# Kernel optimization log

Measured on AMD Instinct MI355X. Metric: run time of the kernel, lower is better.

Reference implementation:

```python
import jax, jax.numpy as jnp
import numpy as np

B, T, D, H, HD, I = 256, 1, 2048, 16, 128, 5504
EPS = 1e-6
ROPE_THETA = 10000.0


def setup_inputs() -> dict:
    key = jax.random.key(0)
    ks = jax.random.split(key, 20)
    W = 0.02  # weight init scale
    hidden_states = jax.random.normal(ks[0], (B, T, D), jnp.float32)
    # RoPE tables for each batch element at a distinct decode position
    pos = jnp.arange(B, dtype=jnp.float32) % 4096.0
    inv_freq = 1.0 / (ROPE_THETA ** (jnp.arange(0, HD, 2, dtype=jnp.float32) / HD))
    ang = pos[:, None] * inv_freq[None, :]                      # [B, HD/2]
    emb = jnp.concatenate([ang, ang], axis=-1)                  # [B, HD]
    cos = jnp.cos(emb)[:, None, :]                              # [B, 1, HD]
    sin = jnp.sin(emb)[:, None, :]
    n = lambda k, s: jax.random.normal(k, s, jnp.float32) * W
    return {
        'hidden_states': hidden_states, 'cos': cos, 'sin': sin,
        'router_w': n(ks[1], (D,)), 'router_b': jnp.zeros((1,), jnp.float32),
        'ln1_w': jnp.ones((D,), jnp.float32), 'ln2_w': jnp.ones((D,), jnp.float32),
        'wq': n(ks[2], (D, D)), 'bq': jnp.zeros((D,), jnp.float32),
        'wk': n(ks[3], (D, D)), 'bk': jnp.zeros((D,), jnp.float32),
        'wv': n(ks[4], (D, D)), 'bv': jnp.zeros((D,), jnp.float32),
        'wo': n(ks[5], (D, D)),
        'w_gate': n(ks[6], (D, I)), 'w_up': n(ks[7], (D, I)), 'w_down': n(ks[8], (I, D)),
        'k_sel': 128,
    }


def _rms(x, w):
    v = jnp.mean(jnp.square(x), axis=-1, keepdims=True)
    return x * jax.lax.rsqrt(v + EPS) * w


def _rotate_half(x):
    x1, x2 = jnp.split(x, 2, axis=-1)
    return jnp.concatenate([-x2, x1], axis=-1)


def _decoder_layer(x, cs, sn, ln1_w, ln2_w, wq, bq, wk, bk, wv, bv, wo, w_gate, w_up, w_down):
    # x: [k, T, D]; cs/sn: [k, T, HD]
    k = x.shape[0]
    h = _rms(x, ln1_w)
    q = (h @ wq + bq).reshape(k, T, H, HD).transpose(0, 2, 1, 3)  # [k,H,T,HD]
    kk = (h @ wk + bk).reshape(k, T, H, HD).transpose(0, 2, 1, 3)
    v = (h @ wv + bv).reshape(k, T, H, HD).transpose(0, 2, 1, 3)
    c = cs[:, None, :, :]  # [k,1,T,HD]
    s = sn[:, None, :, :]
    q = q * c + _rotate_half(q) * s
    kk = kk * c + _rotate_half(kk) * s
    att = jnp.einsum('bhqd,bhkd->bhqk', q, kk) * (HD ** -0.5)
    p = jax.nn.softmax(att, axis=-1)  # T==1: trivial causal mask
    o = jnp.einsum('bhqk,bhkd->bhqd', p, v).transpose(0, 2, 1, 3).reshape(k, T, D) @ wo
    x = x + o
    h2 = _rms(x, ln2_w)
    mlp = (jax.nn.silu(h2 @ w_gate) * (h2 @ w_up)) @ w_down
    return x + mlp


def reference(hidden_states, cos, sin, router_w, router_b, ln1_w, ln2_w,
              wq, bq, wk, bk, wv, bv, wo, w_gate, w_up, w_down, k_sel):
    # causal router: linear D->1 scores per batch row (T==1 decode step)
    scores = hidden_states[:, 0, :] @ router_w + router_b[0]   # [B]
    probs = jax.nn.sigmoid(scores)
    _, sel_idx = jax.lax.top_k(probs, k_sel)                   # [k]
    x_sel = hidden_states[sel_idx]                             # gather [k,T,D]
    cs, sn = cos[sel_idx], sin[sel_idx]                        # [k,T,HD]
    x_out = _decoder_layer(x_sel, cs, sn, ln1_w, ln2_w, wq, bq, wk, bk,
                           wv, bv, wo, w_gate, w_up, w_down)
    return hidden_states.at[sel_idx].set(x_out)                # scatter back
```

## Files before the change

kernel.cpp:

```cpp
#include <hip/hip_runtime.h>
#include <hip/hip_bf16.h>
#include <stdint.h>


#define D_ 2048
#define I_ 5504
#define NROWS 256
#define KSEL 128

typedef __attribute__((ext_vector_type(8))) short short8;
typedef __attribute__((ext_vector_type(4))) float floatx4;

__device__ __forceinline__ unsigned int pk2(float lo, float hi) {
  __hip_bfloat162 h = __float22bfloat162_rn(float2{lo, hi});
  unsigned int u; __builtin_memcpy(&u, &h, 4); return u;
}

__global__ void k_zero(float4* __restrict__ p, int n4) {
  int i = blockIdx.x * 256 + threadIdx.x;
  int st = gridDim.x * 256;
  for (; i < n4; i += st) p[i] = float4{0.f, 0.f, 0.f, 0.f};
}

__global__ void k_router(const float* __restrict__ hid, const float* __restrict__ rw,
                         const float* __restrict__ rb, float* __restrict__ scores) {
  int b = blockIdx.x, t = threadIdx.x;
  const float4* x4 = (const float4*)(hid + (size_t)b * D_);
  const float4* w4 = (const float4*)rw;
  float s = 0.f;
#pragma unroll
  for (int c = 0; c < 2; ++c) {
    float4 xv = x4[t + c * 256], wv = w4[t + c * 256];
    s += xv.x * wv.x + xv.y * wv.y + xv.z * wv.z + xv.w * wv.w;
  }
  for (int o = 32; o; o >>= 1) s += __shfl_down(s, o);
  __shared__ float red[4];
  if ((t & 63) == 0) red[t >> 6] = s;
  __syncthreads();
  if (t == 0) scores[b] = red[0] + red[1] + red[2] + red[3] + rb[0];
}

__global__ void k_select(const float* __restrict__ scores, const int* __restrict__ kptr,
                         int* __restrict__ sel, int* __restrict__ pos) {
  __shared__ float sv[NROWS];
  int t = threadIdx.x;
  sv[t] = scores[t];
  __syncthreads();
  float s = sv[t];
  int c = 0;
  for (int j = 0; j < NROWS; ++j) {
    float o = sv[j];
    c += (o > s) || (o == s && j < t);
  }
  int k = *kptr;
  if (c < k) sel[c] = t;
  pos[t] = (c < k) ? c : -1;
}

__global__ void k_rms1(const float* __restrict__ hid, const int* __restrict__ sel,
                       const float* __restrict__ ln1, const float* __restrict__ bv,
                       unsigned short* __restrict__ Hb, float* __restrict__ V,
                       float* __restrict__ X1) {
  int i = blockIdx.x, t = threadIdx.x;
  int r = sel[i];
  const float4* x4 = (const float4*)(hid + (size_t)r * D_);
  float4 xa = x4[2 * t], xb = x4[2 * t + 1];
  float ss = xa.x * xa.x + xa.y * xa.y + xa.z * xa.z + xa.w * xa.w
           + xb.x * xb.x + xb.y * xb.y + xb.z * xb.z + xb.w * xb.w;
  for (int o = 32; o; o >>= 1) ss += __shfl_down(ss, o);
  __shared__ float red[4];
  if ((t & 63) == 0) red[t >> 6] = ss;
  __syncthreads();
  float inv = rsqrtf((red[0] + red[1] + red[2] + red[3]) * (1.0f / D_) + 1e-6f);
  const float4* w4 = (const float4*)ln1;
  float4 wa = w4[2 * t], wb = w4[2 * t + 1];
  union { unsigned int u[4]; uint4 q; } pk;
  pk.u[0] = pk2(xa.x * inv * wa.x, xa.y * inv * wa.y);
  pk.u[1] = pk2(xa.z * inv * wa.z, xa.w * inv * wa.w);
  pk.u[2] = pk2(xb.x * inv * wb.x, xb.y * inv * wb.y);
  pk.u[3] = pk2(xb.z * inv * wb.z, xb.w * inv * wb.w);
  ((uint4*)(Hb + (size_t)i * D_))[t] = pk.q;
  const float4* b4 = (const float4*)bv;
  float4* V4 = (float4*)(V + (size_t)i * D_);
  V4[2 * t] = b4[2 * t]; V4[2 * t + 1] = b4[2 * t + 1];
  float4* X4 = (float4*)(X1 + (size_t)i * D_);
  X4[2 * t] = xa; X4[2 * t + 1] = xb;
}

__global__ void k_rms2(const float* __restrict__ X1, const float* __restrict__ ln2,
                       unsigned short* __restrict__ H2b) {
  int i = blockIdx.x, t = threadIdx.x;
  const float4* x4 = (const float4*)(X1 + (size_t)i * D_);
  float4 xa = x4[2 * t], xb = x4[2 * t + 1];
  float ss = xa.x * xa.x + xa.y * xa.y + xa.z * xa.z + xa.w * xa.w
           + xb.x * xb.x + xb.y * xb.y + xb.z * xb.z + xb.w * xb.w;
  for (int o = 32; o; o >>= 1) ss += __shfl_down(ss, o);
  __shared__ float red[4];
  if ((t & 63) == 0) red[t >> 6] = ss;
  __syncthreads();
  float inv = rsqrtf((red[0] + red[1] + red[2] + red[3]) * (1.0f / D_) + 1e-6f);
  const float4* w4 = (const float4*)ln2;
  float4 wa = w4[2 * t], wb = w4[2 * t + 1];
  union { unsigned int u[4]; uint4 q; } pk;
  pk.u[0] = pk2(xa.x * inv * wa.x, xa.y * inv * wa.y);
  pk.u[1] = pk2(xa.z * inv * wa.z, xa.w * inv * wa.w);
  pk.u[2] = pk2(xb.x * inv * wb.x, xb.y * inv * wb.y);
  pk.u[3] = pk2(xb.z * inv * wb.z, xb.w * inv * wb.w);
  ((uint4*)(H2b + (size_t)i * D_))[t] = pk.q;
}

__global__ void k_silu_out(const float* __restrict__ G, const float* __restrict__ U,
                           unsigned short* __restrict__ Mb,
                           const float* __restrict__ X1, const int* __restrict__ pos,
                           const float* __restrict__ hid, float* __restrict__ out) {
  int tid = blockIdx.x * 256 + threadIdx.x;
  const int nM4 = KSEL * I_ / 4;
  if (tid < nM4) {
    float4 g = ((const float4*)G)[tid], u = ((const float4*)U)[tid];
    float m0 = (g.x / (1.f + expf(-g.x))) * u.x;
    float m1 = (g.y / (1.f + expf(-g.y))) * u.y;
    float m2 = (g.z / (1.f + expf(-g.z))) * u.z;
    float m3 = (g.w / (1.f + expf(-g.w))) * u.w;
    uint2 o; o.x = pk2(m0, m1); o.y = pk2(m2, m3);
    ((uint2*)Mb)[tid] = o;
  }
  const int nO4 = NROWS * (D_ / 4);
  if (tid < nO4) {
    int row = tid >> 9;
    int c4 = tid & 511;
    int p = pos[row];
    ((float4*)out)[tid] = (p >= 0) ? ((const float4*)X1)[(size_t)p * 512 + c4]
                                   : ((const float4*)hid)[tid];
  }
}

template<bool AF32, bool DUAL>
__global__ __launch_bounds__(256, 2)
void k_gemm(const void* __restrict__ Ap, const float* __restrict__ B0,
            const float* __restrict__ B1, float* __restrict__ C0,
            float* __restrict__ C1, const int* __restrict__ rowmap,
            int K, int KA, int Kb, int lda, int N, int KT, int ldc) {
  constexpr int ST = 72;
  const int bn = blockIdx.x;
  const int kt0 = blockIdx.y * KT;
  const int kt1 = kt0 + KT;
  const int tid = threadIdx.x;
  const int lane = tid & 63;
  const int wave = tid >> 6;
  const int wm = wave >> 1, wn = wave & 1;
  const int fm = lane & 15, kq = lane >> 4;

  __shared__ alignas(16) unsigned short Asm[128 * ST];
  __shared__ alignas(16) unsigned short Bsm0[32 * ST];
  __shared__ alignas(16) unsigned short Bsm1[DUAL ? 32 * ST : 8];

  floatx4 acc0[4] = {};
  floatx4 acc1[4] = {};

  const int arow = tid >> 3;
  const int akg  = (tid & 7) * 8;
  const int frow = tid >> 4;
  const int fkg  = (tid & 15) * 4;
  const int bnn = tid & 31;
  const int bk8 = (tid >> 5) * 8;

  const unsigned short* Ab = AF32 ? nullptr : (const unsigned short*)Ap;
  const float*          Af = AF32 ? (const float*)Ap : nullptr;
  const float* B0c = B0 + (size_t)(bn * 32 + bnn);
  const float* B1c = DUAL ? B1 + (size_t)(bn * 32 + bnn) : nullptr;

  struct Regs {
    uint4 a4[4];
    float4 af8[8];
    float b0v[8], b1v[8];
  };

  auto load_tile = [&](Regs& R, int kt) {
    if constexpr (AF32) {
      const int c0 = kt + fkg;
      const bool ok = c0 < KA;
#pragma unroll
      for (int r = 0; r < 8; ++r) {
        const float* p = Af + (size_t)(r * 16 + frow) * lda + c0;
        R.af8[r] = ok ? *(const float4*)p : make_float4(0.f, 0.f, 0.f, 0.f);
      }
    } else {
      const int c0 = kt + akg;
      const bool ok = c0 < KA;
#pragma unroll
      for (int r = 0; r < 4; ++r) {
        const unsigned short* p = Ab + (size_t)(r * 32 + arow) * lda + c0;
        R.a4[r] = ok ? *(const uint4*)p : make_uint4(0u, 0u, 0u, 0u);
      }
    }
#pragma unroll
    for (int j = 0; j < 8; ++j) {
      int kr = kt + bk8 + j; kr = kr < Kb ? kr : Kb - 1;
      R.b0v[j] = B0c[(size_t)kr * N];
      if constexpr (DUAL) R.b1v[j] = B1c[(size_t)kr * N];
    }
  };

  auto store_lds = [&](Regs& R) {
    if constexpr (AF32) {
#pragma unroll
      for (int r = 0; r < 8; ++r) {
        uint2 w;
        w.x = pk2(R.af8[r].x, R.af8[r].y);
        w.y = pk2(R.af8[r].z, R.af8[r].w);
        *(uint2*)&Asm[(r * 16 + frow) * ST + fkg] = w;
      }
    } else {
#pragma unroll
      for (int r = 0; r < 4; ++r)
        *(uint4*)&Asm[(r * 32 + arow) * ST + akg] = R.a4[r];
    }
    uint4 bq;
    bq.x = pk2(R.b0v[0], R.b0v[1]); bq.y = pk2(R.b0v[2], R.b0v[3]);
    bq.z = pk2(R.b0v[4], R.b0v[5]); bq.w = pk2(R.b0v[6], R.b0v[7]);
    *(uint4*)&Bsm0[bnn * ST + bk8] = bq;
    if constexpr (DUAL) {
      uint4 cq;
      cq.x = pk2(R.b1v[0], R.b1v[1]); cq.y = pk2(R.b1v[2], R.b1v[3]);
      cq.z = pk2(R.b1v[4], R.b1v[5]); cq.w = pk2(R.b1v[6], R.b1v[7]);
      *(uint4*)&Bsm1[bnn * ST + bk8] = cq;
    }
  };

  auto mfma_phase = [&]() {
    short8 afr[2][4], bf0[2], bf1[2];
#pragma unroll
    for (int s = 0; s < 2; ++s) {
#pragma unroll
      for (int i = 0; i < 4; ++i)
        afr[s][i] = *(const short8*)&Asm[(wm * 64 + i * 16 + fm) * ST + s * 32 + kq * 8];
      bf0[s] = *(const short8*)&Bsm0[(wn * 16 + fm) * ST + s * 32 + kq * 8];
      if constexpr (DUAL)
        bf1[s] = *(const short8*)&Bsm1[(wn * 16 + fm) * ST + s * 32 + kq * 8];
    }
#pragma unroll
    for (int s = 0; s < 2; ++s) {
#pragma unroll
      for (int i = 0; i < 4; ++i) {
        acc0[i] = __builtin_amdgcn_mfma_f32_16x16x32_bf16(afr[s][i], bf0[s], acc0[i], 0, 0, 0);
        if constexpr (DUAL)
          acc1[i] = __builtin_amdgcn_mfma_f32_16x16x32_bf16(afr[s][i], bf1[s], acc1[i], 0, 0, 0);
      }
    }
  };

  auto stage = [&](Regs& R, int kt) {
    __builtin_amdgcn_s_barrier();
    __builtin_amdgcn_sched_barrier(0);
    store_lds(R);
    if (kt + 128 < kt1) load_tile(R, kt + 128);
    asm volatile("s_waitcnt lgkmcnt(0)" ::: "memory");
    __builtin_amdgcn_s_barrier();
    __builtin_amdgcn_sched_barrier(0);
    mfma_phase();
    __builtin_amdgcn_sched_barrier(0);
  };

  Regs ra, rb;
  load_tile(ra, kt0);
  load_tile(rb, kt0 + 64);

  int kt = kt0;
  while (true) {
    stage(ra, kt);
    kt += 64; if (kt >= kt1) break;
    stage(rb, kt);
    kt += 64; if (kt >= kt1) break;
  }

#pragma unroll
  for (int i = 0; i < 4; ++i) {
#pragma unroll
    for (int r = 0; r < 4; ++r) {
      int row = wm * 64 + i * 16 + kq * 4 + r;
      size_t rbase = rowmap ? (size_t)rowmap[row] * ldc : (size_t)row * ldc;
      int col = bn * 32 + wn * 16 + fm;
      atomicAdd(&C0[rbase + col], acc0[i][r]);
      if constexpr (DUAL) atomicAdd(&C1[rbase + col], acc1[i][r]);
    }
  }
}

extern "C" void kernel_launch(void* const* d_in, const int* in_sizes, int n_in,
                              void* d_out, int out_size, void* d_ws, size_t ws_size,
                              hipStream_t stream) {
  const float* hid = (const float*)d_in[0];
  const float* rw  = (const float*)d_in[3];
  const float* rb  = (const float*)d_in[4];
  const float* ln1 = (const float*)d_in[5];
  const float* ln2 = (const float*)d_in[6];
  const float* wv  = (const float*)d_in[11];
  const float* bv  = (const float*)d_in[12];
  const float* wo  = (const float*)d_in[13];
  const float* wg  = (const float*)d_in[14];
  const float* wu  = (const float*)d_in[15];
  const float* wd  = (const float*)d_in[16];
  const int*   kp  = (const int*)d_in[17];
  float* out = (float*)d_out;

  char* ws = (char*)d_ws;
  float*          scores = (float*)(ws + 0);
  int*            sel    = (int*)(ws + 1024);
  int*            pos    = (int*)(ws + 1536);
  unsigned short* Hb     = (unsigned short*)(ws + 4096);
  float*          V      = (float*)(ws + 528384);
  float*          X1     = (float*)(ws + 1576960);
  unsigned short* H2b    = (unsigned short*)(ws + 2625536);
  float*          G      = (float*)(ws + 3149824);
  float*          U      = (float*)(ws + 5967872);
  unsigned short* Mb     = (unsigned short*)(ws + 8785920);

  k_zero<<<1024, 256, 0, stream>>>((float4*)G, 352256);
  k_router<<<256, 256, 0, stream>>>(hid, rw, rb, scores);
  k_select<<<1, 256, 0, stream>>>(scores, kp, sel, pos);
  k_rms1<<<128, 256, 0, stream>>>(hid, sel, ln1, bv, Hb, V, X1);
  k_gemm<false, false><<<dim3(64, 8), 256, 0, stream>>>(
      Hb, wv, nullptr, V, nullptr, nullptr, 2048, 2048, 2048, 2048, 2048, 256, 2048);
  k_gemm<true, false><<<dim3(64, 8), 256, 0, stream>>>(
      V, wo, nullptr, X1, nullptr, nullptr, 2048, 2048, 2048, 2048, 2048, 256, 2048);
  k_rms2<<<128, 256, 0, stream>>>(X1, ln2, H2b);
  k_gemm<false, true><<<dim3(172, 4), 256, 0, stream>>>(
      H2b, wg, wu, G, U, nullptr, 2048, 2048, 2048, 2048, 5504, 512, 5504);
  k_silu_out<<<1024, 256, 0, stream>>>(G, U, Mb, X1, pos, hid, out);
  k_gemm<false, false><<<dim3(64, 8), 256, 0, stream>>>(
      Mb, wd, nullptr, out, nullptr, sel, 5632, 5504, 5504, 5504, 2048, 704, 2048);
}
```

Measured before the change: 287.5 us.

## Retile GEMM to 64x128 blocks with XCD-aware block remapping

Changes the GEMM block tile from 128 rows x 32 columns with 64-wide K steps to 64 rows x 128 columns with 32-wide K steps, for wider contiguous weight reads. Splits the M dimension across two blocks and flattens the grid into 1D. Block IDs are remapped so neighbouring tiles land on the same XCD, letting the two M-halves share weight reads in L2. The dual gate/up kernel becomes two separate launches and occupancy is raised to 4 blocks per CU. The cost is that each weight tile is now fetched by two blocks, which only stays cheap if L2 catches the second read, and there are more atomic adds to the output.

```diff
diff --git a/kernel.cpp b/kernel.cpp
--- a/kernel.cpp
+++ b/kernel.cpp
@@ -134,126 +134,113 @@
   }
 }
 
-template<bool AF32, bool DUAL>
-__global__ __launch_bounds__(256, 2)
+template<bool AF32, int NN>
+__global__ __launch_bounds__(256, 4)
 void k_gemm(const void* __restrict__ Ap, const float* __restrict__ B0,
-            const float* __restrict__ B1, float* __restrict__ C0,
-            float* __restrict__ C1, const int* __restrict__ rowmap,
-            int K, int KA, int Kb, int lda, int N, int KT, int ldc) {
-  constexpr int ST = 72;
-  const int bn = blockIdx.x;
-  const int kt0 = blockIdx.y * KT;
+            float* __restrict__ C0, const int* __restrict__ rowmap,
+            int KA, int Kb, int lda, int ldc, int KT, int NT) {
+  constexpr int ST = 40;
+  const int nwg = gridDim.x, id = blockIdx.x;
+  const int q = nwg >> 3, r8 = nwg & 7, xcd = id & 7, lid = id >> 3;
+  const int nid = (xcd < r8 ? xcd * (q + 1) : r8 * (q + 1) + (xcd - r8) * q) + lid;
+  const int bm = nid & 1;
+  const int rest = nid >> 1;
+  const int bn = rest % NT;
+  const int ks = rest / NT;
+  const int kt0 = ks * KT;
   const int kt1 = kt0 + KT;
+
   const int tid = threadIdx.x;
   const int lane = tid & 63;
   const int wave = tid >> 6;
   const int wm = wave >> 1, wn = wave & 1;
   const int fm = lane & 15, kq = lane >> 4;
 
-  __shared__ alignas(16) unsigned short Asm[128 * ST];
-  __shared__ alignas(16) unsigned short Bsm0[32 * ST];
-  __shared__ alignas(16) unsigned short Bsm1[DUAL ? 32 * ST : 8];
-
-  floatx4 acc0[4] = {};
-  floatx4 acc1[4] = {};
-
-  const int arow = tid >> 3;
-  const int akg  = (tid & 7) * 8;
-  const int frow = tid >> 4;
-  const int fkg  = (tid & 15) * 4;
-  const int bnn = tid & 31;
-  const int bk8 = (tid >> 5) * 8;
-
-  const unsigned short* Ab = AF32 ? nullptr : (const unsigned short*)Ap;
-  const float*          Af = AF32 ? (const float*)Ap : nullptr;
-  const float* B0c = B0 + (size_t)(bn * 32 + bnn);
-  const float* B1c = DUAL ? B1 + (size_t)(bn * 32 + bnn) : nullptr;
+  __shared__ alignas(16) unsigned short Asm[64 * ST];
+  __shared__ alignas(16) unsigned short Bsm[128 * ST];
+
+  floatx4 acc[2][4] = {};
+
+  const int ar = tid >> 2;
+  const int acg = (tid & 3) * 8;
+  const int bc = tid & 127;
+  const int bkh = (tid >> 7) * 16;
+
+  const unsigned short* Ab = AF32 ? nullptr
+      : (const unsigned short*)Ap + (size_t)(bm * 64 + ar) * lda + acg;
+  const float* Af = AF32 ? (const float*)Ap + (size_t)(bm * 64 + ar) * lda + acg
+                         : nullptr;
+  int bcg = bn * 128 + bc; if (bcg > NN - 1) bcg = NN - 1;
+  const float* Bc = B0 + bcg;
 
   struct Regs {
-    uint4 a4[4];
-    float4 af8[8];
-    float b0v[8], b1v[8];
+    uint4 a;
+    float4 af[2];
+    float b[16];
   };
 
   auto load_tile = [&](Regs& R, int kt) {
+    const int c0 = kt + acg;
+    const bool ok = c0 < KA;
     if constexpr (AF32) {
-      const int c0 = kt + fkg;
-      const bool ok = c0 < KA;
-#pragma unroll
-      for (int r = 0; r < 8; ++r) {
-        const float* p = Af + (size_t)(r * 16 + frow) * lda + c0;
-        R.af8[r] = ok ? *(const float4*)p : make_float4(0.f, 0.f, 0.f, 0.f);
-      }
+      R.af[0] = ok ? *(const float4*)(Af + kt) : make_float4(0.f, 0.f, 0.f, 0.f);
+      R.af[1] = ok ? *(const float4*)(Af + kt + 4) : make_float4(0.f, 0.f, 0.f, 0.f);
     } else {
-      const int c0 = kt + akg;
-      const bool ok = c0 < KA;
-#pragma unroll
-      for (int r = 0; r < 4; ++r) {
-        const unsigned short* p = Ab + (size_t)(r * 32 + arow) * lda + c0;
-        R.a4[r] = ok ? *(const uint4*)p : make_uint4(0u, 0u, 0u, 0u);
+      R.a = ok ? *(const uint4*)(Ab + kt) : make_uint4(0u, 0u, 0u, 0u);
+    }
+    if (kt + bkh + 15 < Kb) {
+      const float* bp = Bc + (size_t)(kt + bkh) * NN;
+#pragma unroll
+      for (int j = 0; j < 16; ++j) R.b[j] = bp[(size_t)j * NN];
+    } else {
+#pragma unroll
+      for (int j = 0; j < 16; ++j) {
+        int kr = kt + bkh + j; kr = kr < Kb ? kr : Kb - 1;
+        R.b[j] = Bc[(size_t)kr * NN];
       }
     }
-#pragma unroll
-    for (int j = 0; j < 8; ++j) {
-      int kr = kt + bk8 + j; kr = kr < Kb ? kr : Kb - 1;
-      R.b0v[j] = B0c[(size_t)kr * N];
-      if constexpr (DUAL) R.b1v[j] = B1c[(size_t)kr * N];
-    }
   };
 
   auto store_lds = [&](Regs& R) {
     if constexpr (AF32) {
-#pragma unroll
-      for (int r = 0; r < 8; ++r) {
-        uint2 w;
-        w.x = pk2(R.af8[r].x, R.af8[r].y);
-        w.y = pk2(R.af8[r].z, R.af8[r].w);
-        *(uint2*)&Asm[(r * 16 + frow) * ST + fkg] = w;
-      }
+      union { unsigned int u[4]; uint4 qq; } pk;
+      pk.u[0] = pk2(R.af[0].x, R.af[0].y);
+      pk.u[1] = pk2(R.af[0].z, R.af[0].w);
+      pk.u[2] = pk2(R.af[1].x, R.af[1].y);
+      pk.u[3] = pk2(R.af[1].z, R.af[1].w);
+      *(uint4*)&Asm[ar * ST + acg] = pk.qq;
     } else {
-#pragma unroll
-      for (int r = 0; r < 4; ++r)
-        *(uint4*)&Asm[(r * 32 + arow) * ST + akg] = R.a4[r];
+      *(uint4*)&Asm[ar * ST + acg] = R.a;
     }
-    uint4 bq;
-    bq.x = pk2(R.b0v[0], R.b0v[1]); bq.y = pk2(R.b0v[2], R.b0v[3]);
-    bq.z = pk2(R.b0v[4], R.b0v[5]); bq.w = pk2(R.b0v[6], R.b0v[7]);
-    *(uint4*)&Bsm0[bnn * ST + bk8] = bq;
-    if constexpr (DUAL) {
-      uint4 cq;
-      cq.x = pk2(R.b1v[0], R.b1v[1]); cq.y = pk2(R.b1v[2], R.b1v[3]);
-      cq.z = pk2(R.b1v[4], R.b1v[5]); cq.w = pk2(R.b1v[6], R.b1v[7]);
-      *(uint4*)&Bsm1[bnn * ST + bk8] = cq;
-    }
+    union { unsigned int u[4]; uint4 qq; } p0, p1;
+    p0.u[0] = pk2(R.b[0], R.b[1]);   p0.u[1] = pk2(R.b[2], R.b[3]);
+    p0.u[2] = pk2(R.b[4], R.b[5]);   p0.u[3] = pk2(R.b[6], R.b[7]);
+    p1.u[0] = pk2(R.b[8], R.b[9]);   p1.u[1] = pk2(R.b[10], R.b[11]);
+    p1.u[2] = pk2(R.b[12], R.b[13]); p1.u[3] = pk2(R.b[14], R.b[15]);
+    *(uint4*)&Bsm[bc * ST + bkh] = p0.qq;
+    *(uint4*)&Bsm[bc * ST + bkh + 8] = p1.qq;
   };
 
   auto mfma_phase = [&]() {
-    short8 afr[2][4], bf0[2], bf1[2];
-#pragma unroll
-    for (int s = 0; s < 2; ++s) {
-#pragma unroll
-      for (int i = 0; i < 4; ++i)
-        afr[s][i] = *(const short8*)&Asm[(wm * 64 + i * 16 + fm) * ST + s * 32 + kq * 8];
-      bf0[s] = *(const short8*)&Bsm0[(wn * 16 + fm) * ST + s * 32 + kq * 8];
-      if constexpr (DUAL)
-        bf1[s] = *(const short8*)&Bsm1[(wn * 16 + fm) * ST + s * 32 + kq * 8];
-    }
-#pragma unroll
-    for (int s = 0; s < 2; ++s) {
-#pragma unroll
-      for (int i = 0; i < 4; ++i) {
-        acc0[i] = __builtin_amdgcn_mfma_f32_16x16x32_bf16(afr[s][i], bf0[s], acc0[i], 0, 0, 0);
-        if constexpr (DUAL)
-          acc1[i] = __builtin_amdgcn_mfma_f32_16x16x32_bf16(afr[s][i], bf1[s], acc1[i], 0, 0, 0);
-      }
-    }
+    short8 af_[2], bf_[4];
+#pragma unroll
+    for (int i = 0; i < 2; ++i)
+      af_[i] = *(const short8*)&Asm[(wm * 32 + i * 16 + fm) * ST + kq * 8];
+#pragma unroll
+    for (int n = 0; n < 4; ++n)
+      bf_[n] = *(const short8*)&Bsm[(wn * 64 + n * 16 + fm) * ST + kq * 8];
+#pragma unroll
+    for (int i = 0; i < 2; ++i)
+#pragma unroll
+      for (int n = 0; n < 4; ++n)
+        acc[i][n] = __builtin_amdgcn_mfma_f32_16x16x32_bf16(af_[i], bf_[n], acc[i][n], 0, 0, 0);
   };
 
   auto stage = [&](Regs& R, int kt) {
     __builtin_amdgcn_s_barrier();
     __builtin_amdgcn_sched_barrier(0);
     store_lds(R);
-    if (kt + 128 < kt1) load_tile(R, kt + 128);
+    if (kt + 64 < kt1) load_tile(R, kt + 64);
     asm volatile("s_waitcnt lgkmcnt(0)" ::: "memory");
     __builtin_amdgcn_s_barrier();
     __builtin_amdgcn_sched_barrier(0);
@@ -263,25 +250,27 @@
 
   Regs ra, rb;
   load_tile(ra, kt0);
-  load_tile(rb, kt0 + 64);
+  load_tile(rb, kt0 + 32);
 
   int kt = kt0;
   while (true) {
     stage(ra, kt);
-    kt += 64; if (kt >= kt1) break;
+    kt += 32; if (kt >= kt1) break;
     stage(rb, kt);
-    kt += 64; if (kt >= kt1) break;
-  }
-
-#pragma unroll
-  for (int i = 0; i < 4; ++i) {
-#pragma unroll
-    for (int r = 0; r < 4; ++r) {
-      int row = wm * 64 + i * 16 + kq * 4 + r;
-      size_t rbase = rowmap ? (size_t)rowmap[row] * ldc : (size_t)row * ldc;
-      int col = bn * 32 + wn * 16 + fm;
-      atomicAdd(&C0[rbase + col], acc0[i][r]);
-      if constexpr (DUAL) atomicAdd(&C1[rbase + col], acc1[i][r]);
+    kt += 32; if (kt >= kt1) break;
+  }
+
+#pragma unroll
+  for (int i = 0; i < 2; ++i) {
+#pragma unroll
+    for (int n = 0; n < 4; ++n) {
+#pragma unroll
+      for (int rr = 0; rr < 4; ++rr) {
+        int rowl = bm * 64 + wm * 32 + i * 16 + kq * 4 + rr;
+        size_t rbase = rowmap ? (size_t)rowmap[rowl] * ldc : (size_t)rowl * ldc;
+        int col = bn * 128 + wn * 64 + n * 16 + fm;
+        if (col < NN) atomicAdd(&C0[rbase + col], acc[i][n][rr]);
+      }
     }
   }
 }
@@ -319,14 +308,16 @@
   k_router<<<256, 256, 0, stream>>>(hid, rw, rb, scores);
   k_select<<<1, 256, 0, stream>>>(scores, kp, sel, pos);
   k_rms1<<<128, 256, 0, stream>>>(hid, sel, ln1, bv, Hb, V, X1);
-  k_gemm<false, false><<<dim3(64, 8), 256, 0, stream>>>(
-      Hb, wv, nullptr, V, nullptr, nullptr, 2048, 2048, 2048, 2048, 2048, 256, 2048);
-  k_gemm<true, false><<<dim3(64, 8), 256, 0, stream>>>(
-      V, wo, nullptr, X1, nullptr, nullptr, 2048, 2048, 2048, 2048, 2048, 256, 2048);
+  k_gemm<false, 2048><<<512, 256, 0, stream>>>(
+      Hb, wv, V, nullptr, 2048, 2048, 2048, 2048, 128, 16);
+  k_gemm<true, 2048><<<512, 256, 0, stream>>>(
+      V, wo, X1, nullptr, 2048, 2048, 2048, 2048, 128, 16);
   k_rms2<<<128, 256, 0, stream>>>(X1, ln2, H2b);
-  k_gemm<false, true><<<dim3(172, 4), 256, 0, stream>>>(
-      H2b, wg, wu, G, U, nullptr, 2048, 2048, 2048, 2048, 5504, 512, 5504);
+  k_gemm<false, 5504><<<516, 256, 0, stream>>>(
+      H2b, wg, G, nullptr, 2048, 2048, 2048, 5504, 352, 43);
+  k_gemm<false, 5504><<<516, 256, 0, stream>>>(
+      H2b, wu, U, nullptr, 2048, 2048, 2048, 5504, 352, 43);
   k_silu_out<<<1024, 256, 0, stream>>>(G, U, Mb, X1, pos, hid, out);
-  k_gemm<false, false><<<dim3(64, 8), 256, 0, stream>>>(
-      Mb, wd, nullptr, out, nullptr, sel, 5632, 5504, 5504, 5504, 2048, 704, 2048);
-}
+  k_gemm<false, 2048><<<512, 256, 0, stream>>>(
+      Mb, wd, out, sel, 5504, 5504, 5504, 2048, 352, 16);
+}
```

New measurement: 328.0 us. 14.1% more time.
